# Kernel optimization log

Hardware: AMD Instinct MI355X
Metric: run time of the kernel (lower is better)

Reference implementation:

```python
import jax, jax.numpy as jnp
import numpy as np

B = 2048          # batch_size from init
D = 512           # embedding dim
TAU = 0.5         # temperature
EPS = 1e-12       # torch F.normalize eps


def _l2_normalize(x):
    n = jnp.linalg.norm(x, axis=1, keepdims=True)
    return x / jnp.maximum(n, EPS)


def setup_inputs() -> dict:
    key = jax.random.key(0)
    k1, k2 = jax.random.split(key)
    emb_i = jax.random.normal(k1, (2 * B, D), dtype=jnp.float32)
    emb_j = jax.random.normal(k2, (2 * B, D), dtype=jnp.float32)
    return {"emb_i": emb_i, "emb_j": emb_j}


def reference(emb_i, emb_j):
    z_i = _l2_normalize(emb_i)
    z_j = _l2_normalize(emb_j)
    rep = jnp.concatenate([z_i, z_j], axis=0)        # [4B, D], unit rows
    # cosine similarity of unit vectors == plain GEMM
    sim = rep @ rep.T                                # [4B, 4B]
    n = 4 * B
    pos1 = jnp.concatenate([jnp.diagonal(sim, B), jnp.diagonal(sim, -B)])        # [6B]
    pos2 = jnp.concatenate([jnp.diagonal(sim, 2 * B), jnp.diagonal(sim, -2 * B)])  # [4B]
    pos3 = jnp.concatenate([jnp.diagonal(sim, 3 * B), jnp.diagonal(sim, -3 * B)])  # [2B]
    nominator = (jnp.sum(jnp.exp(pos1 / TAU))
                 + jnp.sum(jnp.exp(pos2 / TAU))
                 + jnp.sum(jnp.exp(pos3 / TAU)))
    off_diag = 1.0 - jnp.eye(n, dtype=sim.dtype)
    denominator = jnp.sum(off_diag * jnp.exp(sim / TAU)) - nominator
    loss = -jnp.log(nominator / denominator) / (4 * B)
    return loss
```

## Files before the change

### kernel.cpp

```cpp
#include <hip/hip_runtime.h>
#include <stdint.h>

#define DIM       512
#define NROWS     8192
#define HALF_ROWS 4096
#define TILE      128
#define BK        32

typedef float  floatx4 __attribute__((ext_vector_type(4)));
typedef __bf16 bf16x8  __attribute__((ext_vector_type(8)));

__device__ __forceinline__ void async_copy16(const unsigned short* g, unsigned short* l) {
    __builtin_amdgcn_global_load_lds(
        (const __attribute__((address_space(1))) uint32_t*)(g),
        (__attribute__((address_space(3))) uint32_t*)(l),
        16, 0, 0);
}

__global__ void init_ws(double* ws) {
    ws[0] = 0.0;
    ws[1] = 0.0;
}

__global__ __launch_bounds__(256) void normalize_kernel(
    const float* __restrict__ emb_i, const float* __restrict__ emb_j,
    unsigned short* __restrict__ rep)
{
    const int wave = threadIdx.x >> 6;
    const int lane = threadIdx.x & 63;
    const int row  = blockIdx.x * 4 + wave;
    const float* src = (row < HALF_ROWS) ? (emb_i + (size_t)row * DIM)
                                         : (emb_j + (size_t)(row - HALF_ROWS) * DIM);
    const int c = lane * 8;
    float4 v0 = *(const float4*)(src + c);
    float4 v1 = *(const float4*)(src + c + 4);
    float s = v0.x*v0.x + v0.y*v0.y + v0.z*v0.z + v0.w*v0.w
            + v1.x*v1.x + v1.y*v1.y + v1.z*v1.z + v1.w*v1.w;
    #pragma unroll
    for (int off = 32; off; off >>= 1) s += __shfl_xor(s, off, 64);
    const float nrm = sqrtf(s);
    const float inv = 1.0f / fmaxf(nrm, 1e-12f);
    float f[8] = {v0.x*inv, v0.y*inv, v0.z*inv, v0.w*inv,
                  v1.x*inv, v1.y*inv, v1.z*inv, v1.w*inv};
    union { unsigned short h[8]; uint4 u; } pk;
    #pragma unroll
    for (int t = 0; t < 8; ++t) {
        uint32_t b = __float_as_uint(f[t]);
        b += 0x7FFFu + ((b >> 16) & 1u);
        pk.h[t] = (unsigned short)(b >> 16);
    }
    *(uint4*)(rep + (size_t)row * DIM + c) = pk.u;
}

__global__ __launch_bounds__(256) void gram_kernel(
    const unsigned short* __restrict__ rep, double* __restrict__ ws)
{
    const int bj = blockIdx.x, bi = blockIdx.y;
    if (bj < bi) return;

    __shared__ unsigned short As[TILE * BK];
    __shared__ unsigned short Bs[TILE * BK];
    __shared__ float red[8];

    const int tid  = threadIdx.x;
    const int wave = tid >> 6, lane = tid & 63;
    const int wm = wave >> 1, wn = wave & 1;
    const int m = lane & 15, quad = lane >> 4;

    floatx4 acc[4][4];
    #pragma unroll
    for (int a = 0; a < 4; ++a)
        #pragma unroll
        for (int b = 0; b < 4; ++b)
            #pragma unroll
            for (int e = 0; e < 4; ++e) acc[a][b][e] = 0.0f;

    const int i0 = bi * TILE, j0 = bj * TILE;

    for (int k0 = 0; k0 < DIM; k0 += BK) {
        #pragma unroll
        for (int r = 0; r < 2; ++r) {
            const int chunk = r * 256 + tid;
            const int row   = chunk >> 2;
            const int cc    = (chunk & 3) * 8;
            async_copy16(rep + (size_t)(i0 + row) * DIM + k0 + cc, As + chunk * 8);
            async_copy16(rep + (size_t)(j0 + row) * DIM + k0 + cc, Bs + chunk * 8);
        }
        __syncthreads();

        bf16x8 af[4], bfr[4];
        #pragma unroll
        for (int mt = 0; mt < 4; ++mt)
            af[mt] = *(const bf16x8*)(As + (wm * 64 + mt * 16 + m) * BK + quad * 8);
        #pragma unroll
        for (int nt = 0; nt < 4; ++nt)
            bfr[nt] = *(const bf16x8*)(Bs + (wn * 64 + nt * 16 + m) * BK + quad * 8);
        #pragma unroll
        for (int mt = 0; mt < 4; ++mt)
            #pragma unroll
            for (int nt = 0; nt < 4; ++nt)
                acc[mt][nt] = __builtin_amdgcn_mfma_f32_16x16x32_bf16(
                    af[mt], bfr[nt], acc[mt][nt], 0, 0, 0);
        __syncthreads();
    }

    float s_all = 0.0f, s_pos = 0.0f;
    const float LOG2E2 = 2.885390081777927f;
    #pragma unroll
    for (int mt = 0; mt < 4; ++mt) {
        const int ibase = i0 + wm * 64 + mt * 16 + quad * 4;
        #pragma unroll
        for (int nt = 0; nt < 4; ++nt) {
            const int j = j0 + wn * 64 + nt * 16 + m;
            const floatx4 a = acc[mt][nt];
            #pragma unroll
            for (int r2 = 0; r2 < 4; ++r2) {
                const int i = ibase + r2;
                const float e = exp2f(a[r2] * LOG2E2);
                if (i != j) s_all += e;
                const int d = j - i;
                if (d == 2048 || d == 4096 || d == 6144) s_pos += e;
            }
        }
    }
    #pragma unroll
    for (int off = 32; off; off >>= 1) {
        s_all += __shfl_xor(s_all, off, 64);
        s_pos += __shfl_xor(s_pos, off, 64);
    }
    if (lane == 0) { red[wave] = s_all; red[4 + wave] = s_pos; }
    __syncthreads();
    if (tid == 0) {
        const float w  = (bi == bj) ? 1.0f : 2.0f;
        const float ta = (red[0] + red[1] + red[2] + red[3]) * w;
        const float tp = (red[4] + red[5] + red[6] + red[7]) * w;
        atomicAdd(&ws[0], (double)ta);
        atomicAdd(&ws[1], (double)tp);
    }
}

__global__ void finalize_kernel(const double* __restrict__ ws, float* __restrict__ out) {
    const double nom = ws[1];
    const double den = ws[0] - nom;
    out[0] = (float)(-log(nom / den) / (double)NROWS);
}

extern "C" void kernel_launch(void* const* d_in, const int* in_sizes, int n_in,
                              void* d_out, int out_size, void* d_ws, size_t ws_size,
                              hipStream_t stream) {
    const float* emb_i = (const float*)d_in[0];
    const float* emb_j = (const float*)d_in[1];
    float* out = (float*)d_out;
    double* ws = (double*)d_ws;
    unsigned short* rep = (unsigned short*)((char*)d_ws + 256);

    hipLaunchKernelGGL(init_ws, dim3(1), dim3(1), 0, stream, ws);
    hipLaunchKernelGGL(normalize_kernel, dim3(NROWS / 4), dim3(256), 0, stream,
                       emb_i, emb_j, rep);
    hipLaunchKernelGGL(gram_kernel, dim3(64, 64), dim3(256), 0, stream, rep, ws);
    hipLaunchKernelGGL(finalize_kernel, dim3(1), dim3(1), 0, stream, ws, out);
}
```

Before: 148.3 us.

## Swizzle LDS tiles, launch only upper-triangle blocks, fuse init and finalize

The LDS tile layout is XOR-swizzled on both the async global-to-LDS copy and the MFMA fragment reads, to reduce bank conflicts. The 64x64 grid, where half the blocks exit at once, becomes a 1D grid of 2080 upper-triangle tiles decoded from a linear index. The init and finalize kernels are folded away: normalize zeroes the workspace, and the last gram block, found via an atomic counter, computes the loss, which saves two launches. In exchange each block does a sqrt-based index decode and the counter adds a fence and an extra atomic per block.

```diff
diff --git a/kernel.cpp b/kernel.cpp
--- a/kernel.cpp
+++ b/kernel.cpp
@@ -6,6 +6,8 @@
 #define HALF_ROWS 4096
 #define TILE      128
 #define BK        32
+#define NTILE     64
+#define NBLK      2080
 
 typedef float  floatx4 __attribute__((ext_vector_type(4)));
 typedef __bf16 bf16x8  __attribute__((ext_vector_type(8)));
@@ -17,15 +19,15 @@
         16, 0, 0);
 }
 
-__global__ void init_ws(double* ws) {
-    ws[0] = 0.0;
-    ws[1] = 0.0;
-}
-
 __global__ __launch_bounds__(256) void normalize_kernel(
     const float* __restrict__ emb_i, const float* __restrict__ emb_j,
-    unsigned short* __restrict__ rep)
+    unsigned short* __restrict__ rep, double* __restrict__ ws)
 {
+    if (blockIdx.x == 0 && threadIdx.x == 0) {
+        ws[0] = 0.0;
+        ws[1] = 0.0;
+        *(unsigned int*)((char*)ws + 16) = 0u;
+    }
     const int wave = threadIdx.x >> 6;
     const int lane = threadIdx.x & 63;
     const int row  = blockIdx.x * 4 + wave;
@@ -53,10 +55,14 @@
 }
 
 __global__ __launch_bounds__(256) void gram_kernel(
-    const unsigned short* __restrict__ rep, double* __restrict__ ws)
+    const unsigned short* __restrict__ rep, double* __restrict__ ws,
+    float* __restrict__ out)
 {
-    const int bj = blockIdx.x, bi = blockIdx.y;
-    if (bj < bi) return;
+    const int ell = blockIdx.x;
+    int bj = (int)((sqrt(8.0 * (double)ell + 1.0) - 1.0) * 0.5);
+    while ((bj + 1) * (bj + 2) / 2 <= ell) ++bj;
+    while (bj * (bj + 1) / 2 > ell) --bj;
+    const int bi = ell - bj * (bj + 1) / 2;
 
     __shared__ unsigned short As[TILE * BK];
     __shared__ unsigned short Bs[TILE * BK];
@@ -66,6 +72,7 @@
     const int wave = tid >> 6, lane = tid & 63;
     const int wm = wave >> 1, wn = wave & 1;
     const int m = lane & 15, quad = lane >> 4;
+    const int sw = (quad ^ ((m >> 1) & 3)) * 8;
 
     floatx4 acc[4][4];
     #pragma unroll
@@ -77,24 +84,23 @@
 
     const int i0 = bi * TILE, j0 = bj * TILE;
 
+    const int p0 = tid,      r0 = p0 >> 2, jj0 = ((p0 & 3) ^ ((r0 >> 1) & 3)) * 8;
+    const int p1 = 256 + tid, r1 = p1 >> 2, jj1 = ((p1 & 3) ^ ((r1 >> 1) & 3)) * 8;
+
     for (int k0 = 0; k0 < DIM; k0 += BK) {
-        #pragma unroll
-        for (int r = 0; r < 2; ++r) {
-            const int chunk = r * 256 + tid;
-            const int row   = chunk >> 2;
-            const int cc    = (chunk & 3) * 8;
-            async_copy16(rep + (size_t)(i0 + row) * DIM + k0 + cc, As + chunk * 8);
-            async_copy16(rep + (size_t)(j0 + row) * DIM + k0 + cc, Bs + chunk * 8);
-        }
+        async_copy16(rep + (size_t)(i0 + r0) * DIM + k0 + jj0, As + p0 * 8);
+        async_copy16(rep + (size_t)(j0 + r0) * DIM + k0 + jj0, Bs + p0 * 8);
+        async_copy16(rep + (size_t)(i0 + r1) * DIM + k0 + jj1, As + p1 * 8);
+        async_copy16(rep + (size_t)(j0 + r1) * DIM + k0 + jj1, Bs + p1 * 8);
         __syncthreads();
 
         bf16x8 af[4], bfr[4];
         #pragma unroll
         for (int mt = 0; mt < 4; ++mt)
-            af[mt] = *(const bf16x8*)(As + (wm * 64 + mt * 16 + m) * BK + quad * 8);
+            af[mt] = *(const bf16x8*)(As + (wm * 64 + mt * 16 + m) * BK + sw);
         #pragma unroll
         for (int nt = 0; nt < 4; ++nt)
-            bfr[nt] = *(const bf16x8*)(Bs + (wn * 64 + nt * 16 + m) * BK + quad * 8);
+            bfr[nt] = *(const bf16x8*)(Bs + (wn * 64 + nt * 16 + m) * BK + sw);
         #pragma unroll
         for (int mt = 0; mt < 4; ++mt)
             #pragma unroll
@@ -136,13 +142,17 @@
         const float tp = (red[4] + red[5] + red[6] + red[7]) * w;
         atomicAdd(&ws[0], (double)ta);
         atomicAdd(&ws[1], (double)tp);
+        __threadfence();
+        unsigned int* cnt = (unsigned int*)((char*)ws + 16);
+        const unsigned int prev = atomicAdd(cnt, 1u);
+        if (prev == NBLK - 1) {
+            __threadfence();
+            const double tot = atomicAdd(&ws[0], 0.0);
+            const double nom = atomicAdd(&ws[1], 0.0);
+            const double den = tot - nom;
+            out[0] = (float)(-log(nom / den) / (double)NROWS);
+        }
     }
-}
-
-__global__ void finalize_kernel(const double* __restrict__ ws, float* __restrict__ out) {
-    const double nom = ws[1];
-    const double den = ws[0] - nom;
-    out[0] = (float)(-log(nom / den) / (double)NROWS);
 }
 
 extern "C" void kernel_launch(void* const* d_in, const int* in_sizes, int n_in,
@@ -154,9 +164,7 @@
     double* ws = (double*)d_ws;
     unsigned short* rep = (unsigned short*)((char*)d_ws + 256);
 
-    hipLaunchKernelGGL(init_ws, dim3(1), dim3(1), 0, stream, ws);
     hipLaunchKernelGGL(normalize_kernel, dim3(NROWS / 4), dim3(256), 0, stream,
-                       emb_i, emb_j, rep);
-    hipLaunchKernelGGL(gram_kernel, dim3(64, 64), dim3(256), 0, stream, rep, ws);
-    hipLaunchKernelGGL(finalize_kernel, dim3(1), dim3(1), 0, stream, ws, out);
+                       emb_i, emb_j, rep, ws);
+    hipLaunchKernelGGL(gram_kernel, dim3(NBLK), dim3(256), 0, stream, rep, ws, out);
 }
```

Result: slower. 177.7 us (+19.8%).
